# Optimization experiments

Hardware: AMD Instinct MI355X
Metric: run time of the kernel (lower is better)

Reference implementation:

```python
import jax, jax.numpy as jnp
import numpy as np


def _mlp2(x, W1, b1, W2, b2):
    # two-layer MLP with ReLU hidden activation
    h = jax.nn.relu(jnp.einsum('...i,ij->...j', x, W1) + b1)
    return jnp.einsum('...i,ij->...j', h, W2) + b2


def setup_inputs() -> dict:
    key = jax.random.key(0)
    ks = jax.random.split(key, 8)
    B, N, D = 8, 256, 64
    positions = jax.random.normal(ks[0], (B, N, 3), dtype=jnp.float32)
    values = jax.random.normal(ks[1], (B, N, D), dtype=jnp.float32)
    # value_net: 2 -> D -> D ; score_net: D -> D -> 1 (He-style init)
    Wv1 = jax.random.normal(ks[2], (2, D), dtype=jnp.float32) * np.sqrt(2.0 / 2)
    bv1 = jnp.zeros((D,), dtype=jnp.float32)
    Wv2 = jax.random.normal(ks[3], (D, D), dtype=jnp.float32) * np.sqrt(2.0 / D)
    bv2 = jnp.zeros((D,), dtype=jnp.float32)
    Ws1 = jax.random.normal(ks[4], (D, D), dtype=jnp.float32) * np.sqrt(2.0 / D)
    bs1 = jnp.zeros((D,), dtype=jnp.float32)
    Ws2 = jax.random.normal(ks[5], (D, 1), dtype=jnp.float32) * np.sqrt(2.0 / D)
    bs2 = jnp.zeros((1,), dtype=jnp.float32)
    return dict(positions=positions, values=values, Wv1=Wv1, bv1=bv1, Wv2=Wv2,
                bv2=bv2, Ws1=Ws1, bs1=bs1, Ws2=Ws2, bs2=bs2)


def reference(positions, values, Wv1, bv1, Wv2, bv2, Ws1, bs1, Ws2, bs2):
    # rank-2 geometric algebra attention, reduce=True, merge_fun=join_fun='mean'
    B, N, _ = positions.shape
    r_i = positions[:, :, None, :]            # [B, N, 1, 3]
    r_j = positions[:, None, :, :]            # [B, 1, N, 3]
    # geometric product of two vectors -> scalar (dot) + bivector (wedge)
    dot = jnp.sum(r_i * r_j, axis=-1)         # [B, N, N] scalar part
    wedge = jnp.cross(r_i, r_j)               # [B, N, N, 3] bivector components
    biv_norm = jnp.sqrt(jnp.sum(wedge * wedge, axis=-1) + 1e-20)
    invariants = jnp.stack([dot, biv_norm], axis=-1)             # [B, N, N, 2]
    # merge_fun='mean' over the pair of node values
    merged = 0.5 * (values[:, :, None, :] + values[:, None, :, :])  # [B,N,N,D]
    invar_values = _mlp2(invariants, Wv1, bv1, Wv2, bv2)            # [B,N,N,D]
    # join_fun='mean' of value_net(invariants) and merged node values
    joined = 0.5 * (invar_values + merged)                          # [B,N,N,D]
    scores = _mlp2(joined, Ws1, bs1, Ws2, bs2)                      # [B,N,N,1]
    # reduce=True: softmax over all N*N product indices, output is [B, D]
    attn = jax.nn.softmax(scores.reshape(B, N * N), axis=-1).reshape(B, N, N, 1)
    output = jnp.sum(attn * joined, axis=(1, 2))                    # [B, D]
    return output
```

## Files before the change

kernel.cpp:

```cpp
#include <hip/hip_runtime.h>
#include <hip/hip_bf16.h>

#define NB 8
#define NN 256
#define DD 64

#define OFF_WCSW  0
#define OFF_CSA   2048
#define OFF_CSB   3072
#define OFF_CSC   4096
#define OFF_CC    5120
#define OFF_MI    5184
#define OFF_RSI   7232
#define OFF_U     9280
#define OFF_SHR   140352

typedef __attribute__((ext_vector_type(4))) float f32x4;
typedef __attribute__((ext_vector_type(8))) short s16x8;

static __device__ __forceinline__ unsigned short bf16_rn(float x) {
    unsigned u = __float_as_uint(x);
    u += 0x8000u;
    return (unsigned short)(u >> 16);
}

__global__ __launch_bounds__(256) void k_setup(
    const float* __restrict__ values, const float* __restrict__ Wv1,
    const float* __restrict__ bv1, const float* __restrict__ Wv2,
    const float* __restrict__ bv2, const float* __restrict__ Ws1,
    const float* __restrict__ bs1, float* __restrict__ ws)
{
    int idx = blockIdx.x * 256 + threadIdx.x;
    if (idx < 131072) {
        int d = idx & 63;
        const float* v = values + (idx >> 6) * 64;
        float s = 0.f;
#pragma unroll 8
        for (int k = 0; k < 64; k++) s = fmaf(v[k], Ws1[k * 64 + d], s);
        ws[OFF_U + idx] = 0.25f * s;
    } else if (idx < 135168) {
        int e = idx - 131072;
        int j = e & 7, ln = (e >> 3) & 63, nt = (e >> 9) & 3, ks = e >> 11;
        int k = ks * 32 + ((ln >> 4) & 3) * 8 + j;
        int d = nt * 16 + (ln & 15);
        float s = 0.f;
#pragma unroll 8
        for (int m = 0; m < 64; m++) s = fmaf(Wv2[k * 64 + m], Ws1[m * 64 + d], s);
        ((unsigned short*)(ws + OFF_WCSW))[e] = bf16_rn(0.5f * s);
    } else if (idx < 136192) {
        int e = idx - 135168;
        int j = e & 7, ln = (e >> 3) & 63, ks = e >> 9;
        int k = ks * 32 + ((ln >> 4) & 3) * 8 + j;
        ws[OFF_CSA + e] = Wv1[k];
        ws[OFF_CSB + e] = Wv1[64 + k];
        ws[OFF_CSC + e] = bv1[k];
    } else if (idx < 136256) {
        int d = idx - 136192;
        float s = 0.f;
#pragma unroll 8
        for (int k = 0; k < 64; k++) s = fmaf(bv2[k], Ws1[k * 64 + d], s);
        ws[OFF_CC + d] = 0.5f * s + bs1[d];
    }
}

__global__ __launch_bounds__(256, 2) void k_main(
    const float* __restrict__ pos, const float* __restrict__ Wv1,
    const float* __restrict__ bv1, const float* __restrict__ Ws2,
    float* __restrict__ ws)
{
    __shared__ float2 ldsDB[2 * 256];
    __shared__ float  ldsS[2][256];
    __shared__ float  ldsCCU[2 * 64];
    __shared__ float  ldsWs2[64];
    __shared__ float  ldsPos[6];
    __shared__ float  ldsRed[4];
    __shared__ float  ldsP[4][64];

    int b  = blockIdx.x >> 7;
    int i0 = (blockIdx.x & 127) * 2;
    int t  = threadIdx.x;
    int lane = t & 63, wv = t >> 6;
    const float* uB = ws + OFF_U + b * (NN * DD);

    if (t < 6)  ldsPos[t] = pos[(b * 256 + i0) * 3 + t];
    if (t < 64) ldsWs2[t] = Ws2[t];
    if (t < 128) {
        int ii = t >> 6, d = t & 63;
        ldsCCU[t] = ws[OFF_CC + d] + uB[(i0 + ii) * 64 + d];
    }
    __syncthreads();

    {
        float px = pos[(b * 256 + t) * 3 + 0];
        float py = pos[(b * 256 + t) * 3 + 1];
        float pz = pos[(b * 256 + t) * 3 + 2];
#pragma unroll
        for (int ii = 0; ii < 2; ii++) {
            float ax = ldsPos[ii * 3 + 0], ay = ldsPos[ii * 3 + 1], az = ldsPos[ii * 3 + 2];
            float dot = ax * px + ay * py + az * pz;
            float cx = ay * pz - az * py;
            float cy = az * px - ax * pz;
            float cz = ax * py - ay * px;
            float biv = sqrtf(cx * cx + cy * cy + cz * cz + 1e-20f);
            ldsDB[ii * 256 + t] = make_float2(dot, biv);
        }
    }
    __syncthreads();

    int q = lane >> 4, col = lane & 15;

    float cA[16], cB[16], cC[16];
    {
        const f32x4* pa0 = (const f32x4*)(ws + OFF_CSA + lane * 8);
        const f32x4* pa1 = (const f32x4*)(ws + OFF_CSA + 512 + lane * 8);
        ((f32x4*)cA)[0] = pa0[0]; ((f32x4*)cA)[1] = pa0[1];
        ((f32x4*)cA)[2] = pa1[0]; ((f32x4*)cA)[3] = pa1[1];
        const f32x4* pb0 = (const f32x4*)(ws + OFF_CSB + lane * 8);
        const f32x4* pb1 = (const f32x4*)(ws + OFF_CSB + 512 + lane * 8);
        ((f32x4*)cB)[0] = pb0[0]; ((f32x4*)cB)[1] = pb0[1];
        ((f32x4*)cB)[2] = pb1[0]; ((f32x4*)cB)[3] = pb1[1];
        const f32x4* pc0 = (const f32x4*)(ws + OFF_CSC + lane * 8);
        const f32x4* pc1 = (const f32x4*)(ws + OFF_CSC + 512 + lane * 8);
        ((f32x4*)cC)[0] = pc0[0]; ((f32x4*)cC)[1] = pc0[1];
        ((f32x4*)cC)[2] = pc1[0]; ((f32x4*)cC)[3] = pc1[1];
    }
    s16x8 bfr[2][4];
    {
        const s16x8* wsw = (const s16x8*)(ws + OFF_WCSW);
#pragma unroll
        for (int ks = 0; ks < 2; ks++)
#pragma unroll
            for (int nt = 0; nt < 4; nt++)
                bfr[ks][nt] = wsw[(ks * 4 + nt) * 64 + lane];
    }

#pragma unroll
    for (int jt4 = 0; jt4 < 4; jt4++) {
        int jt = wv * 4 + jt4;
        float uc[4][4];
#pragma unroll
        for (int r = 0; r < 4; r++) {
            int jl = jt * 16 + q * 4 + r;
#pragma unroll
            for (int nt = 0; nt < 4; nt++)
                uc[r][nt] = uB[jl * 64 + nt * 16 + col];
        }
#pragma unroll
        for (int ii = 0; ii < 2; ii++) {
            float2 db = ldsDB[ii * 256 + jt * 16 + col];
            s16x8 af[2];
#pragma unroll
            for (int ks = 0; ks < 2; ks++)
#pragma unroll
                for (int j = 0; j < 8; j++) {
                    float h = fmaf(db.x, cA[ks * 8 + j], fmaf(db.y, cB[ks * 8 + j], cC[ks * 8 + j]));
                    af[ks][j] = (short)bf16_rn(fmaxf(h, 0.f));
                }
            f32x4 acc[4];
#pragma unroll
            for (int nt = 0; nt < 4; nt++) acc[nt] = (f32x4){0.f, 0.f, 0.f, 0.f};
#pragma unroll
            for (int nt = 0; nt < 4; nt++) {
                acc[nt] = __builtin_amdgcn_mfma_f32_16x16x32_bf16(af[0], bfr[0][nt], acc[nt], 0, 0, 0);
                acc[nt] = __builtin_amdgcn_mfma_f32_16x16x32_bf16(af[1], bfr[1][nt], acc[nt], 0, 0, 0);
            }
            float tr[4] = {0.f, 0.f, 0.f, 0.f};
#pragma unroll
            for (int nt = 0; nt < 4; nt++) {
                float cu = ldsCCU[ii * 64 + nt * 16 + col];
                float w2 = ldsWs2[nt * 16 + col];
#pragma unroll
                for (int r = 0; r < 4; r++) {
                    float s = acc[nt][r] + cu + uc[r][nt];
                    tr[r] = fmaf(fmaxf(s, 0.f), w2, tr[r]);
                }
            }
#pragma unroll
            for (int m = 1; m < 16; m <<= 1) {
#pragma unroll
                for (int r = 0; r < 4; r++) tr[r] += __shfl_xor(tr[r], m);
            }
            if (col == 0) {
                float4 sc4 = make_float4(tr[0], tr[1], tr[2], tr[3]);
                *(float4*)&ldsS[ii][jt * 16 + q * 4] = sc4;
            }
        }
    }
    __syncthreads();

    float A = Wv1[lane], B = Wv1[64 + lane], C = bv1[lane];
#pragma unroll
    for (int ii = 0; ii < 2; ii++) {
        float sv = ldsS[ii][t];
        float wm = sv;
#pragma unroll
        for (int md = 1; md < 64; md <<= 1) wm = fmaxf(wm, __shfl_xor(wm, md));
        if (lane == 0) ldsRed[wv] = wm;
        __syncthreads();
        float m_row = fmaxf(fmaxf(ldsRed[0], ldsRed[1]), fmaxf(ldsRed[2], ldsRed[3]));
        float wgt = __expf(sv - m_row);
        float rsp = wgt;
#pragma unroll
        for (int md = 1; md < 64; md <<= 1) rsp += __shfl_xor(rsp, md);
        __syncthreads();
        if (lane == 0) ldsRed[wv] = rsp;
        __syncthreads();
        float rowsum = ldsRed[0] + ldsRed[1] + ldsRed[2] + ldsRed[3];

        float acc = 0.f;
#pragma unroll 8
        for (int jj = 0; jj < 64; jj++) {
            float w = __shfl(wgt, jj);
            float2 db = ldsDB[ii * 256 + wv * 64 + jj];
            float h = fmaxf(fmaf(db.x, A, fmaf(db.y, B, C)), 0.f);
            acc = fmaf(w, h, acc);
        }
        ldsP[wv][lane] = acc;
        __syncthreads();
        int row = b * 256 + i0 + ii;
        if (t < 64)
            ws[OFF_SHR + row * 64 + t] = ldsP[0][t] + ldsP[1][t] + ldsP[2][t] + ldsP[3][t];
        if (t == 0) { ws[OFF_MI + row] = m_row; ws[OFF_RSI + row] = rowsum; }
        __syncthreads();
    }
}

__global__ __launch_bounds__(256) void k_final(
    const float* __restrict__ values, const float* __restrict__ Wv2,
    const float* __restrict__ bv2, const float* __restrict__ ws,
    float* __restrict__ out)
{
    __shared__ float scl[256], zl[256], red[4], pS[4][64], pA[4][64], shv[64], a2v[64];
    int b = blockIdx.x, t = threadIdx.x, wv = t >> 6, lane = t & 63;

    float mi = ws[OFF_MI + b * 256 + t];
    float wm = mi;
#pragma unroll
    for (int md = 1; md < 64; md <<= 1) wm = fmaxf(wm, __shfl_xor(wm, md));
    if (lane == 0) red[wv] = wm;
    __syncthreads();
    float M = fmaxf(fmaxf(red[0], red[1]), fmaxf(red[2], red[3]));

    float rs = ws[OFF_RSI + b * 256 + t];
    float sc = __expf(mi - M);
    float zt = sc * rs;
    scl[t] = sc; zl[t] = zt;
    float zp = zt;
#pragma unroll
    for (int md = 1; md < 64; md <<= 1) zp += __shfl_xor(zp, md);
    __syncthreads();
    if (lane == 0) red[wv] = zp;
    __syncthreads();
    float Z = red[0] + red[1] + red[2] + red[3];

    float accS = 0.f, accA = 0.f;
    const float* shrB = ws + OFF_SHR + b * 256 * 64;
    const float* vB   = values + b * 256 * 64;
#pragma unroll 4
    for (int jj = 0; jj < 64; jj++) {
        int row = wv * 64 + jj;
        accS = fmaf(scl[row], shrB[row * 64 + lane], accS);
        accA = fmaf(zl[row],  vB[row * 64 + lane],  accA);
    }
    pS[wv][lane] = accS; pA[wv][lane] = accA;
    __syncthreads();
    if (t < 64) {
        shv[t] = pS[0][t] + pS[1][t] + pS[2][t] + pS[3][t];
        a2v[t] = pA[0][t] + pA[1][t] + pA[2][t] + pA[3][t];
    }
    __syncthreads();
    if (t < 64) {
        float t1 = 0.f;
#pragma unroll 8
        for (int k = 0; k < 64; k++) t1 = fmaf(shv[k], Wv2[k * 64 + t], t1);
        out[b * 64 + t] = 0.5f * (t1 + a2v[t]) / Z + 0.5f * bv2[t];
    }
}

extern "C" void kernel_launch(void* const* d_in, const int* in_sizes, int n_in,
                              void* d_out, int out_size, void* d_ws, size_t ws_size,
                              hipStream_t stream)
{
    const float* positions = (const float*)d_in[0];
    const float* values    = (const float*)d_in[1];
    const float* Wv1       = (const float*)d_in[2];
    const float* bv1       = (const float*)d_in[3];
    const float* Wv2       = (const float*)d_in[4];
    const float* bv2       = (const float*)d_in[5];
    const float* Ws1       = (const float*)d_in[6];
    const float* bs1       = (const float*)d_in[7];
    const float* Ws2       = (const float*)d_in[8];
    float* ws  = (float*)d_ws;
    float* out = (float*)d_out;

    k_setup<<<533, 256, 0, stream>>>(values, Wv1, bv1, Wv2, bv2, Ws1, bs1, ws);
    k_main<<<1024, 256, 0, stream>>>(positions, Wv1, bv1, Ws2, ws);
    k_final<<<NB, 256, 0, stream>>>(values, Wv2, bv2, ws, out);
}
```

Before: 109.2 us.

## Fold values@Ws1 projection into main MFMA loop with fp16 operands

Stops precomputing the U = values·Ws1 table in the setup kernel. The main kernel now feeds fp16 values and a fp16 Ws1 tile held in LDS straight into extra MFMAs alongside the value-net GEMM. The first-layer value-net activations are computed in packed fp16 vector arithmetic, the operand type switches from bf16 to fp16, and occupancy is raised to 4 blocks per CU. This removes a large fp32 table write/read and the per-element uc loads, at the cost of doubling MFMA work per tile and some fp16 precision risk.

```diff
diff --git a/kernel.cpp b/kernel.cpp
--- a/kernel.cpp
+++ b/kernel.cpp
@@ -1,28 +1,22 @@
 #include <hip/hip_runtime.h>
 #include <hip/hip_bf16.h>
+#include <hip/hip_fp16.h>
 
 #define NB 8
 #define NN 256
 #define DD 64
 
-#define OFF_WCSW  0
-#define OFF_CSA   2048
-#define OFF_CSB   3072
-#define OFF_CSC   4096
-#define OFF_CC    5120
-#define OFF_MI    5184
-#define OFF_RSI   7232
-#define OFF_U     9280
-#define OFF_SHR   140352
+#define OFF_WCF   0
+#define OFF_W1F   2048
+#define OFF_CSF   4096
+#define OFF_CC    5632
+#define OFF_MI    5696
+#define OFF_RSI   7744
+#define OFF_SHR   9792
+#define OFF_VF    140864
 
 typedef __attribute__((ext_vector_type(4))) float f32x4;
-typedef __attribute__((ext_vector_type(8))) short s16x8;
-
-static __device__ __forceinline__ unsigned short bf16_rn(float x) {
-    unsigned u = __float_as_uint(x);
-    u += 0x8000u;
-    return (unsigned short)(u >> 16);
-}
+typedef _Float16 f16x8 __attribute__((ext_vector_type(8)));
 
 __global__ __launch_bounds__(256) void k_setup(
     const float* __restrict__ values, const float* __restrict__ Wv1,
@@ -32,30 +26,33 @@
 {
     int idx = blockIdx.x * 256 + threadIdx.x;
     if (idx < 131072) {
-        int d = idx & 63;
-        const float* v = values + (idx >> 6) * 64;
-        float s = 0.f;
-#pragma unroll 8
-        for (int k = 0; k < 64; k++) s = fmaf(v[k], Ws1[k * 64 + d], s);
-        ws[OFF_U + idx] = 0.25f * s;
+        ((_Float16*)(ws + OFF_VF))[idx] = (_Float16)values[idx];
     } else if (idx < 135168) {
         int e = idx - 131072;
         int j = e & 7, ln = (e >> 3) & 63, nt = (e >> 9) & 3, ks = e >> 11;
-        int k = ks * 32 + ((ln >> 4) & 3) * 8 + j;
+        int k = ks * 32 + (ln >> 4) * 8 + j;
         int d = nt * 16 + (ln & 15);
         float s = 0.f;
 #pragma unroll 8
         for (int m = 0; m < 64; m++) s = fmaf(Wv2[k * 64 + m], Ws1[m * 64 + d], s);
-        ((unsigned short*)(ws + OFF_WCSW))[e] = bf16_rn(0.5f * s);
-    } else if (idx < 136192) {
+        ((_Float16*)(ws + OFF_WCF))[e] = (_Float16)(0.5f * s);
+    } else if (idx < 139264) {
         int e = idx - 135168;
-        int j = e & 7, ln = (e >> 3) & 63, ks = e >> 9;
-        int k = ks * 32 + ((ln >> 4) & 3) * 8 + j;
-        ws[OFF_CSA + e] = Wv1[k];
-        ws[OFF_CSB + e] = Wv1[64 + k];
-        ws[OFF_CSC + e] = bv1[k];
-    } else if (idx < 136256) {
-        int d = idx - 136192;
+        int j = e & 7, ln = (e >> 3) & 63, nt = (e >> 9) & 3, ks = e >> 11;
+        int k = ks * 32 + (ln >> 4) * 8 + j;
+        int d = nt * 16 + (ln & 15);
+        ((_Float16*)(ws + OFF_W1F))[e] = (_Float16)(0.25f * Ws1[k * 64 + d]);
+    } else if (idx < 142336) {
+        int e = idx - 139264;
+        int ln = e / 48;
+        int rem = e - ln * 48;
+        int coef = rem >> 4, kslot = rem & 15;
+        int ks = kslot >> 3, j = kslot & 7;
+        int k = ks * 32 + (ln >> 4) * 8 + j;
+        float v = (coef == 0) ? Wv1[k] : (coef == 1) ? Wv1[64 + k] : bv1[k];
+        ((_Float16*)(ws + OFF_CSF))[ln * 48 + coef * 16 + kslot] = (_Float16)v;
+    } else if (idx < 142400) {
+        int d = idx - 142336;
         float s = 0.f;
 #pragma unroll 8
         for (int k = 0; k < 64; k++) s = fmaf(bv2[k], Ws1[k * 64 + d], s);
@@ -63,30 +60,53 @@
     }
 }
 
-__global__ __launch_bounds__(256, 2) void k_main(
+__global__ __launch_bounds__(256, 4) void k_main(
     const float* __restrict__ pos, const float* __restrict__ Wv1,
     const float* __restrict__ bv1, const float* __restrict__ Ws2,
     float* __restrict__ ws)
 {
-    __shared__ float2 ldsDB[2 * 256];
-    __shared__ float  ldsS[2][256];
-    __shared__ float  ldsCCU[2 * 64];
-    __shared__ float  ldsWs2[64];
-    __shared__ float  ldsPos[6];
-    __shared__ float  ldsRed[4];
-    __shared__ float  ldsP[4][64];
+    __shared__ float2   ldsDB[2 * 256];
+    __shared__ float    ldsS[2][256];
+    __shared__ float    ldsCCU[2 * 64];
+    __shared__ float    ldsWs2[64];
+    __shared__ float    ldsPos[6];
+    __shared__ float    ldsRed[4];
+    __shared__ float    ldsP[4][64];
+    __shared__ _Float16 ldsW1[4096];
 
     int b  = blockIdx.x >> 7;
     int i0 = (blockIdx.x & 127) * 2;
     int t  = threadIdx.x;
     int lane = t & 63, wv = t >> 6;
-    const float* uB = ws + OFF_U + b * (NN * DD);
-
+    int q = lane >> 4, col = lane & 15;
+
+    const _Float16* vf = (const _Float16*)(ws + OFF_VF);
+
+    {
+        const float4* src = (const float4*)(ws + OFF_W1F);
+        float4* dst = (float4*)ldsW1;
+        dst[t] = src[t];
+        dst[256 + t] = src[256 + t];
+    }
     if (t < 6)  ldsPos[t] = pos[(b * 256 + i0) * 3 + t];
     if (t < 64) ldsWs2[t] = Ws2[t];
-    if (t < 128) {
-        int ii = t >> 6, d = t & 63;
-        ldsCCU[t] = ws[OFF_CC + d] + uB[(i0 + ii) * 64 + d];
+    if (t < 128) ldsCCU[t] = ws[OFF_CC + (t & 63)];
+
+    f16x8 cfA[2], cfB[2], cfC[2];
+    {
+        const f16x8* cs = (const f16x8*)((const _Float16*)(ws + OFF_CSF) + lane * 48);
+        cfA[0] = cs[0]; cfA[1] = cs[1];
+        cfB[0] = cs[2]; cfB[1] = cs[3];
+        cfC[0] = cs[4]; cfC[1] = cs[5];
+    }
+    f16x8 wcf[2][4];
+    {
+        const f16x8* p = (const f16x8*)(ws + OFF_WCF);
+#pragma unroll
+        for (int ks = 0; ks < 2; ks++)
+#pragma unroll
+            for (int nt = 0; nt < 4; nt++)
+                wcf[ks][nt] = p[(ks * 4 + nt) * 64 + lane];
     }
     __syncthreads();
 
@@ -105,64 +125,66 @@
             ldsDB[ii * 256 + t] = make_float2(dot, biv);
         }
     }
-    __syncthreads();
-
-    int q = lane >> 4, col = lane & 15;
-
-    float cA[16], cB[16], cC[16];
-    {
-        const f32x4* pa0 = (const f32x4*)(ws + OFF_CSA + lane * 8);
-        const f32x4* pa1 = (const f32x4*)(ws + OFF_CSA + 512 + lane * 8);
-        ((f32x4*)cA)[0] = pa0[0]; ((f32x4*)cA)[1] = pa0[1];
-        ((f32x4*)cA)[2] = pa1[0]; ((f32x4*)cA)[3] = pa1[1];
-        const f32x4* pb0 = (const f32x4*)(ws + OFF_CSB + lane * 8);
-        const f32x4* pb1 = (const f32x4*)(ws + OFF_CSB + 512 + lane * 8);
-        ((f32x4*)cB)[0] = pb0[0]; ((f32x4*)cB)[1] = pb0[1];
-        ((f32x4*)cB)[2] = pb1[0]; ((f32x4*)cB)[3] = pb1[1];
-        const f32x4* pc0 = (const f32x4*)(ws + OFF_CSC + lane * 8);
-        const f32x4* pc1 = (const f32x4*)(ws + OFF_CSC + 512 + lane * 8);
-        ((f32x4*)cC)[0] = pc0[0]; ((f32x4*)cC)[1] = pc0[1];
-        ((f32x4*)cC)[2] = pc1[0]; ((f32x4*)cC)[3] = pc1[1];
-    }
-    s16x8 bfr[2][4];
-    {
-        const s16x8* wsw = (const s16x8*)(ws + OFF_WCSW);
-#pragma unroll
-        for (int ks = 0; ks < 2; ks++)
-#pragma unroll
-            for (int nt = 0; nt < 4; nt++)
-                bfr[ks][nt] = wsw[(ks * 4 + nt) * 64 + lane];
-    }
+
+    if (wv == 0) {
+        const f16x8* w1 = (const f16x8*)ldsW1;
+        f16x8 afu[2];
+#pragma unroll
+        for (int ks = 0; ks < 2; ks++) {
+            if (col < 2)
+                afu[ks] = ((const f16x8*)(vf + (b * 256 + i0 + col) * 64))[ks * 4 + q];
+            else
+                afu[ks] = (f16x8)(_Float16)0.f;
+        }
+        f32x4 ua[4];
+#pragma unroll
+        for (int nt = 0; nt < 4; nt++) {
+            ua[nt] = (f32x4){0.f, 0.f, 0.f, 0.f};
+            ua[nt] = __builtin_amdgcn_mfma_f32_16x16x32_f16(afu[0], w1[(0 * 4 + nt) * 64 + lane], ua[nt], 0, 0, 0);
+            ua[nt] = __builtin_amdgcn_mfma_f32_16x16x32_f16(afu[1], w1[(1 * 4 + nt) * 64 + lane], ua[nt], 0, 0, 0);
+        }
+        if (q == 0) {
+#pragma unroll
+            for (int nt = 0; nt < 4; nt++) {
+#pragma unroll
+                for (int r = 0; r < 2; r++)
+                    ldsCCU[r * 64 + nt * 16 + col] += ua[nt][r];
+            }
+        }
+    }
+    __syncthreads();
+
+    const f16x8* w1 = (const f16x8*)ldsW1;
 
 #pragma unroll
     for (int jt4 = 0; jt4 < 4; jt4++) {
         int jt = wv * 4 + jt4;
-        float uc[4][4];
-#pragma unroll
-        for (int r = 0; r < 4; r++) {
-            int jl = jt * 16 + q * 4 + r;
-#pragma unroll
-            for (int nt = 0; nt < 4; nt++)
-                uc[r][nt] = uB[jl * 64 + nt * 16 + col];
-        }
+        f16x8 av[2];
+#pragma unroll
+        for (int ks = 0; ks < 2; ks++)
+            av[ks] = ((const f16x8*)(vf + (b * 256 + jt * 16 + col) * 64))[ks * 4 + q];
+
 #pragma unroll
         for (int ii = 0; ii < 2; ii++) {
             float2 db = ldsDB[ii * 256 + jt * 16 + col];
-            s16x8 af[2];
-#pragma unroll
-            for (int ks = 0; ks < 2; ks++)
-#pragma unroll
-                for (int j = 0; j < 8; j++) {
-                    float h = fmaf(db.x, cA[ks * 8 + j], fmaf(db.y, cB[ks * 8 + j], cC[ks * 8 + j]));
-                    af[ks][j] = (short)bf16_rn(fmaxf(h, 0.f));
-                }
+            _Float16 dh = (_Float16)db.x, bh = (_Float16)db.y;
+            f16x8 d8, b8;
+#pragma unroll
+            for (int p = 0; p < 8; p++) { d8[p] = dh; b8[p] = bh; }
+            f16x8 af[2];
+#pragma unroll
+            for (int ks = 0; ks < 2; ks++) {
+                f16x8 h = d8 * cfA[ks] + b8 * cfB[ks] + cfC[ks];
+                af[ks] = __builtin_elementwise_max(h, (f16x8)(_Float16)0.f);
+            }
             f32x4 acc[4];
 #pragma unroll
-            for (int nt = 0; nt < 4; nt++) acc[nt] = (f32x4){0.f, 0.f, 0.f, 0.f};
-#pragma unroll
             for (int nt = 0; nt < 4; nt++) {
-                acc[nt] = __builtin_amdgcn_mfma_f32_16x16x32_bf16(af[0], bfr[0][nt], acc[nt], 0, 0, 0);
-                acc[nt] = __builtin_amdgcn_mfma_f32_16x16x32_bf16(af[1], bfr[1][nt], acc[nt], 0, 0, 0);
+                acc[nt] = (f32x4){0.f, 0.f, 0.f, 0.f};
+                acc[nt] = __builtin_amdgcn_mfma_f32_16x16x32_f16(av[0], w1[(0 * 4 + nt) * 64 + lane], acc[nt], 0, 0, 0);
+                acc[nt] = __builtin_amdgcn_mfma_f32_16x16x32_f16(av[1], w1[(1 * 4 + nt) * 64 + lane], acc[nt], 0, 0, 0);
+                acc[nt] = __builtin_amdgcn_mfma_f32_16x16x32_f16(af[0], wcf[0][nt], acc[nt], 0, 0, 0);
+                acc[nt] = __builtin_amdgcn_mfma_f32_16x16x32_f16(af[1], wcf[1][nt], acc[nt], 0, 0, 0);
             }
             float tr[4] = {0.f, 0.f, 0.f, 0.f};
 #pragma unroll
@@ -171,7 +193,7 @@
                 float w2 = ldsWs2[nt * 16 + col];
 #pragma unroll
                 for (int r = 0; r < 4; r++) {
-                    float s = acc[nt][r] + cu + uc[r][nt];
+                    float s = acc[nt][r] + cu;
                     tr[r] = fmaf(fmaxf(s, 0.f), w2, tr[r]);
                 }
             }
@@ -202,6 +224,7 @@
         float rsp = wgt;
 #pragma unroll
         for (int md = 1; md < 64; md <<= 1) rsp += __shfl_xor(rsp, md);
+        ldsS[ii][t] = wgt;
         __syncthreads();
         if (lane == 0) ldsRed[wv] = rsp;
         __syncthreads();
@@ -210,8 +233,9 @@
         float acc = 0.f;
 #pragma unroll 8
         for (int jj = 0; jj < 64; jj++) {
-            float w = __shfl(wgt, jj);
-            float2 db = ldsDB[ii * 256 + wv * 64 + jj];
+            int j = wv * 64 + jj;
+            float w = ldsS[ii][j];
+            float2 db = ldsDB[ii * 256 + j];
             float h = fmaxf(fmaf(db.x, A, fmaf(db.y, B, C)), 0.f);
             acc = fmaf(w, h, acc);
         }
@@ -293,7 +317,7 @@
     float* ws  = (float*)d_ws;
     float* out = (float*)d_out;
 
-    k_setup<<<533, 256, 0, stream>>>(values, Wv1, bv1, Wv2, bv2, Ws1, bs1, ws);
+    k_setup<<<557, 256, 0, stream>>>(values, Wv1, bv1, Wv2, bv2, Ws1, bs1, ws);
     k_main<<<1024, 256, 0, stream>>>(positions, Wv1, bv1, Ws2, ws);
     k_final<<<NB, 256, 0, stream>>>(values, Wv2, bv2, ws, out);
 }
```

Measured after the change: 105.6 us. -3.4%, faster.
